# Kernel tuning notes

Measured on AMD Instinct MI355X. Metric: run time of the kernel, lower is better.

## Reference

```python
import jax, jax.numpy as jnp
import numpy as np
import math

L, B, T, D, H, DH, DM, V = 4, 1, 2048, 1024, 16, 64, 4096, 32000
K_TOP = 512
EPS = 1e-6


def setup_inputs() -> dict:
    key = jax.random.key(0)
    ks = jax.random.split(key, 8)
    s = 0.02
    sp = 0.02 / math.sqrt(2 * L)  # c_proj special init
    return {
        "idx": jax.random.randint(ks[0], (B, T), 0, V),
        "wte": jax.random.normal(ks[1], (V, D), jnp.float32) * s,
        "wpe": jax.random.normal(ks[2], (T, D), jnp.float32) * s,
        "ln1_w": jnp.ones((L, D), jnp.float32),
        "ln2_w": jnp.ones((L, D), jnp.float32),
        "W_attn": jax.random.normal(ks[3], (L, D, 3 * H * DH), jnp.float32) * s,
        "W_attn_proj": jax.random.normal(ks[4], (L, H * DH, D), jnp.float32) * sp,
        "W_fc": jax.random.normal(ks[5], (L, D, DM), jnp.float32) * s,
        "W_mlp_proj": jax.random.normal(ks[6], (L, DM, D), jnp.float32) * sp,
        "sink_logit": jnp.zeros((L, H), jnp.float32),
        "lnf_w": jnp.ones((D,), jnp.float32),
        "lm_head_w": jax.random.normal(ks[7], (D, V), jnp.float32) * s,
        "k_topk": K_TOP,
    }


def rmsnorm(x, w):
    return x * jax.lax.rsqrt(jnp.mean(x * x, axis=-1, keepdims=True) + EPS) * w


def abs_topk(x, k):
    # zero all but the k largest-magnitude entries along the last axis
    if k >= x.shape[-1]:
        return x
    vals = jax.lax.top_k(jnp.abs(x), k)[0]
    thresh = vals[..., -1:]
    return jnp.where(jnp.abs(x) >= thresh, x, jnp.zeros((), x.dtype))


def attention_with_sink(xn, Wa, Wap, sink, causal):
    b, t, _ = xn.shape
    qkv = xn @ Wa  # [B,T,3*H*DH]
    q, k, v = jnp.split(qkv, 3, axis=-1)
    q = q.reshape(b, t, H, DH).transpose(0, 2, 1, 3)  # [B,H,T,DH]
    k = k.reshape(b, t, H, DH).transpose(0, 2, 1, 3)
    v = v.reshape(b, t, H, DH).transpose(0, 2, 1, 3)
    scale = 1.0 / math.sqrt(DH)
    scores = jnp.einsum('bhqd,bhkd->bhqk', q, k) * scale
    neg = jnp.finfo(scores.dtype).min
    scores = jnp.where(causal, scores, neg)
    # sink: zero key/value slot at position 0, logit = per-head learnable bias
    sink_col = jnp.broadcast_to(sink[None, :, None, None], (b, H, t, 1)).astype(scores.dtype)
    logits = jnp.concatenate([sink_col, scores], axis=-1)  # [B,H,T,T+1]
    probs = jax.nn.softmax(logits, axis=-1)
    y = jnp.einsum('bhqk,bhkd->bhqd', probs[..., 1:], v)  # sink v is zero
    y = y.transpose(0, 2, 1, 3).reshape(b, t, H * DH)
    return y @ Wap


def reference(idx, wte, wpe, ln1_w, ln2_w, W_attn, W_attn_proj, W_fc, W_mlp_proj,
              sink_logit, lnf_w, lm_head_w, k_topk):
    b, t = idx.shape
    x = wte[idx] + wpe[jnp.arange(t)][None]  # [B,T,D]
    causal = jnp.tril(jnp.ones((t, t), bool))

    def block(x, p):
        l1, l2, Wa, Wap, Wf, Wp, sk = p
        x = x + attention_with_sink(rmsnorm(x, l1), Wa, Wap, sk, causal)
        h = jax.nn.gelu(rmsnorm(x, l2) @ Wf, approximate=False)
        h = abs_topk(h, k_topk)  # AbsTopK at 'mlp_neuron'
        x = x + h @ Wp
        return x, None

    x, _ = jax.lax.scan(block, x, (ln1_w, ln2_w, W_attn, W_attn_proj, W_fc, W_mlp_proj, sink_logit))
    return rmsnorm(x, lnf_w) @ lm_head_w  # [B,T,V]
```

## Files before the change

### kernel.cpp

```cpp
#include <hip/hip_runtime.h>


typedef unsigned int u32;

#define TT 2048
#define DD 1024
#define HH 16
#define DMM 4096
#define VV 32000
#define AQ 4

__global__ __launch_bounds__(256) void embed32_k(const int* __restrict__ idx,
    const float* __restrict__ wte, const float* __restrict__ wpe, float* __restrict__ x){
  int t = blockIdx.x, tid = threadIdx.x;
  int tok = idx[t];
  #pragma unroll
  for (int i=0;i<4;i++){
    int e = tid*4 + i;
    x[(size_t)t*DD + e] = __fadd_rn(wte[(size_t)tok*DD + e], wpe[(size_t)t*DD + e]);
  }
}

__global__ __launch_bounds__(64) void rms_xla_k(const float* __restrict__ x,
    const float* __restrict__ w, float* __restrict__ out){
  __shared__ float sq[1024];
  __shared__ float p5[512];
  __shared__ float fin[64];
  __shared__ float srt;
  int row = blockIdx.x, lane = threadIdx.x;
  const float* xr = x + (size_t)row*DD;
  for (int i=lane; i<1024; i+=64){ float v = xr[i]; sq[i] = __fmul_rn(v,v); }
  __syncthreads();
  for (int t=lane; t<512; t+=64)
    p5[t] = __fadd_rn(sq[2*t], sq[2*t+1]);
  __syncthreads();
  #pragma unroll
  for (int off=32; off; off>>=1){
    for (int t=lane; t<8*off; t+=64){
      int wv = t/off, ii = t - wv*off;
      p5[64*wv+ii] = __fadd_rn(p5[64*wv+ii], p5[64*wv+ii+off]);
    }
    __syncthreads();
  }
  fin[lane] = (lane<8) ? p5[64*lane] : 0.0f;
  __syncthreads();
  #pragma unroll
  for (int off=32; off; off>>=1){
    if (lane<off) fin[lane] = __fadd_rn(fin[lane], fin[lane+off]);
    __syncthreads();
  }
  if (lane==0){
    float mean = __fdiv_rn(fin[0], 1024.0f);
    srt = rsqrtf(__fadd_rn(mean, 1e-6f));
  }
  __syncthreads();
  float r = srt;
  for (int i=lane; i<1024; i+=64)
    out[(size_t)row*DD + i] = __fmul_rn(__fmul_rn(xr[i], r), w[i]);
}

template<int MODE, int NQ>
__global__ __launch_bounds__(256) void gemm_db_k(const float* __restrict__ A,
    const float* __restrict__ B, float* __restrict__ C, int M, int N, int K){
  __shared__ float As[2][16][132];
  __shared__ float Bs[2][16][64*NQ+4];
  const int tid = threadIdx.x;
  const int tr = tid >> 4, tc = tid & 15;
  const int m0 = blockIdx.y*128, n0 = blockIdx.x*(64*NQ);

  const int ar0 = tid >> 2,       af0 = tid & 3;
  const int ar1 = (256+tid) >> 2, af1 = tid & 3;
  float acc[8][4*NQ];
  #pragma unroll
  for (int i=0;i<8;i++)
    #pragma unroll
    for (int j=0;j<4*NQ;j++) acc[i][j] = 0.0f;

  const int niter = K >> 4;
  {
    float4 va0 = *(const float4*)&A[(size_t)(m0+ar0)*K + 4*af0];
    float4 va1 = *(const float4*)&A[(size_t)(m0+ar1)*K + 4*af1];
    As[0][4*af0+0][ar0]=va0.x; As[0][4*af0+1][ar0]=va0.y; As[0][4*af0+2][ar0]=va0.z; As[0][4*af0+3][ar0]=va0.w;
    As[0][4*af1+0][ar1]=va1.x; As[0][4*af1+1][ar1]=va1.y; As[0][4*af1+2][ar1]=va1.z; As[0][4*af1+3][ar1]=va1.w;
    if (NQ==2){
      int r0 = tid>>5, c40 = tid&31;
      int r1 = (256+tid)>>5, c41 = tid&31;
      *(float4*)&Bs[0][r0][4*c40] = *(const float4*)&B[(size_t)r0*N + n0 + 4*c40];
      *(float4*)&Bs[0][r1][4*c41] = *(const float4*)&B[(size_t)r1*N + n0 + 4*c41];
    } else {
      int r0 = tid>>4, c40 = tid&15;
      *(float4*)&Bs[0][r0][4*c40] = *(const float4*)&B[(size_t)r0*N + n0 + 4*c40];
    }
  }
  __syncthreads();

  for (int t=0; t<niter; ++t){
    const int cur = t & 1;
    float4 va0, va1, vb0, vb1;
    if (t+1 < niter){
      int kk = (t+1) << 4;
      va0 = *(const float4*)&A[(size_t)(m0+ar0)*K + kk + 4*af0];
      va1 = *(const float4*)&A[(size_t)(m0+ar1)*K + kk + 4*af1];
      if (NQ==2){
        int r0 = tid>>5, c40 = tid&31;
        int r1 = (256+tid)>>5;
        vb0 = *(const float4*)&B[(size_t)(kk+r0)*N + n0 + 4*c40];
        vb1 = *(const float4*)&B[(size_t)(kk+r1)*N + n0 + 4*c40];
      } else {
        int r0 = tid>>4, c40 = tid&15;
        vb0 = *(const float4*)&B[(size_t)(kk+r0)*N + n0 + 4*c40];
      }
    }
    #pragma unroll 4
    for (int k=0; k<16; ++k){
      float4 a0 = *(const float4*)&As[cur][k][4*tr];
      float4 a1 = *(const float4*)&As[cur][k][64 + 4*tr];
      float4 b0 = *(const float4*)&Bs[cur][k][4*tc];
      float av[8] = {a0.x,a0.y,a0.z,a0.w, a1.x,a1.y,a1.z,a1.w};
      float bv[4*NQ];
      bv[0]=b0.x; bv[1]=b0.y; bv[2]=b0.z; bv[3]=b0.w;
      if (NQ==2){
        float4 b1 = *(const float4*)&Bs[cur][k][64 + 4*tc];
        bv[4]=b1.x; bv[5]=b1.y; bv[6]=b1.z; bv[7]=b1.w;
      }
      #pragma unroll
      for (int i=0;i<8;i++)
        #pragma unroll
        for (int j=0;j<4*NQ;j++)
          acc[i][j] = __builtin_fmaf(av[i], bv[j], acc[i][j]);
    }
    if (t+1 < niter){
      const int nxt = cur ^ 1;
      As[nxt][4*af0+0][ar0]=va0.x; As[nxt][4*af0+1][ar0]=va0.y; As[nxt][4*af0+2][ar0]=va0.z; As[nxt][4*af0+3][ar0]=va0.w;
      As[nxt][4*af1+0][ar1]=va1.x; As[nxt][4*af1+1][ar1]=va1.y; As[nxt][4*af1+2][ar1]=va1.z; As[nxt][4*af1+3][ar1]=va1.w;
      if (NQ==2){
        int r0 = tid>>5, c40 = tid&31;
        int r1 = (256+tid)>>5;
        *(float4*)&Bs[nxt][r0][4*c40] = vb0;
        *(float4*)&Bs[nxt][r1][4*c40] = vb1;
      } else {
        int r0 = tid>>4, c40 = tid&15;
        *(float4*)&Bs[nxt][r0][4*c40] = vb0;
      }
    }
    __syncthreads();
  }

  #pragma unroll
  for (int i=0;i<8;i++){
    int row = m0 + (i>>2)*64 + 4*tr + (i&3);
    #pragma unroll
    for (int jq=0;jq<NQ;jq++){
      size_t off = (size_t)row*N + n0 + jq*64 + 4*tc;
      #pragma unroll
      for (int e=0;e<4;e++){
        float vv = acc[i][jq*4+e];
        if (MODE==0){
          C[off+e] = vv;
        } else if (MODE==1){
          C[off+e] = __fadd_rn(C[off+e], vv);
        } else {
          float t2 = __fdiv_rn(vv, 1.41421356f);
          float g = erff(t2);
          C[off+e] = __fmul_rn(__fmul_rn(0.5f, vv), __fadd_rn(1.0f, g));
        }
      }
    }
  }
}

__global__ __launch_bounds__(256) void attn_v5_k(const float* __restrict__ qkv,
    const float* __restrict__ sink, float* __restrict__ y){
  __shared__ float arr[AQ][2052];
  __shared__ float uks[64*68];
  __shared__ float mq[AQ];
  __shared__ float dq[AQ];
  float (*Ks)[68]   = (float(*)[68])uks;
  float (*p5)[512]  = (float(*)[512])uks;
  float (*fin)[64]  = (float(*)[64])(uks + AQ*512);
  const int tid = threadIdx.x;
  const int lane = tid & 63, wv = tid >> 6;
  const int h = blockIdx.y, q0 = blockIdx.x*AQ;
  const int qa_w = q0 + wv;
  const float snk = sink[h];

  #pragma unroll
  for (int qi=0;qi<AQ;qi++)
    for (int s=tid; s<2052; s+=256) arr[qi][s] = 0.0f;

  float qv[64];
  {
    const float* qr = qkv + (size_t)qa_w*3072 + h*64;
    #pragma unroll
    for (int c4=0;c4<16;c4++){
      float4 v = *(const float4*)&qr[4*c4];
      qv[4*c4]=v.x; qv[4*c4+1]=v.y; qv[4*c4+2]=v.z; qv[4*c4+3]=v.w;
    }
  }

  float ml = -3.402823466e38f;
  const int qmax = q0 + AQ - 1;
  for (int base=0; base<=qmax; base+=64){
    __syncthreads();
    #pragma unroll
    for (int it=0; it<4; ++it){
      int id = it*256 + tid;
      int r = id >> 4, c4 = id & 15;
      int kr = base + r;
      if (kr < TT)
        *(float4*)&Ks[r][4*c4] = *(const float4*)&qkv[(size_t)kr*3072 + 1024 + h*64 + 4*c4];
    }
    __syncthreads();
    int kv = base + lane;
    if (kv <= qa_w){
      float s = 0.0f;
      #pragma unroll
      for (int c4=0;c4<16;c4++){
        float4 kf = *(const float4*)&Ks[lane][4*c4];
        s = __builtin_fmaf(qv[4*c4  ], kf.x, s);
        s = __builtin_fmaf(qv[4*c4+1], kf.y, s);
        s = __builtin_fmaf(qv[4*c4+2], kf.z, s);
        s = __builtin_fmaf(qv[4*c4+3], kf.w, s);
      }
      s = __fmul_rn(s, 0.125f);
      arr[wv][1+kv] = s;
      ml = fmaxf(ml, s);
    }
  }
  #pragma unroll
  for (int off=1; off<64; off<<=1) ml = fmaxf(ml, __shfl_xor(ml, off, 64));
  if (lane==0) mq[wv] = fmaxf(ml, snk);
  __syncthreads();

  #pragma unroll
  for (int qi=0;qi<AQ;qi++){
    float m = mq[qi]; int qa = q0+qi;
    for (int s=tid; s<2049; s+=256){
      if (s >= 1 && s-1 <= qa)
        arr[qi][s] = expf(__fsub_rn(arr[qi][s], m));
    }
  }
  if (tid < AQ) arr[tid][0] = expf(__fsub_rn(snk, mq[tid]));
  __syncthreads();

  #pragma unroll
  for (int m2=0; m2<8; ++m2){
    int flat = m2*256 + tid;
    int qi = flat >> 9, t = flat & 511;
    float a = 0.0f;
    for (int s=t; s<2049; s+=512) a = __fadd_rn(a, arr[qi][s]);
    p5[qi][t] = a;
  }
  __syncthreads();
  #pragma unroll
  for (int off=32; off; off>>=1){
    for (int t=tid; t<AQ*8*off; t+=256){
      int qi = t/(8*off); int rem = t - qi*8*off;
      int g = rem/off, ii = rem - g*off;
      p5[qi][64*g+ii] = __fadd_rn(p5[qi][64*g+ii], p5[qi][64*g+ii+off]);
    }
    __syncthreads();
  }
  { int qi = tid>>6, i = tid&63; fin[qi][i] = (i<8) ? p5[qi][64*i] : 0.0f; }
  __syncthreads();
  #pragma unroll
  for (int off=32; off; off>>=1){
    for (int t=tid; t<AQ*off; t+=256){
      int qi = t/off, ii = t - qi*off;
      fin[qi][ii] = __fadd_rn(fin[qi][ii], fin[qi][ii+off]);
    }
    __syncthreads();
  }
  if (tid < AQ) dq[tid] = fin[tid][0];
  __syncthreads();

  #pragma unroll
  for (int qi=0;qi<AQ;qi++){
    float den = dq[qi]; int qa = q0+qi;
    for (int s=tid; s<2049; s+=256)
      if (s >= 1 && s-1 <= qa)
        arr[qi][s] = __fdiv_rn(arr[qi][s], den);
  }
  __syncthreads();

  const int d = lane;
  float acc = 0.0f;
  const float* vb = qkv + 2048 + h*64 + d;
  int kv = 0;
  for (; kv + 8 <= qa_w + 1; kv += 8){
    #pragma unroll
    for (int e=0;e<8;e++)
      acc = __builtin_fmaf(arr[wv][1+kv+e], vb[(size_t)(kv+e)*3072], acc);
  }
  for (; kv <= qa_w; ++kv)
    acc = __builtin_fmaf(arr[wv][1+kv], vb[(size_t)kv*3072], acc);
  y[(size_t)qa_w*DD + h*64 + d] = acc;
}

__global__ __launch_bounds__(256) void topk32_k(float* __restrict__ h,
    const int* __restrict__ kptr){
  const int row = blockIdx.x, tid = threadIdx.x;
  __shared__ int suf[256];
  __shared__ int s_sel, s_k;
  float* hr = h + (size_t)row*DMM;
  int kk = kptr[0];
  u32 prefix = 0u;
  for (int pass=0; pass<4; pass++){
    int shift = 24 - 8*pass;
    u32 hi_mask = pass ? (0xFFFFFFFFu << (shift+8)) : 0u;
    suf[tid] = 0;
    __syncthreads();
    for (int i=0;i<16;i++){
      u32 b = __float_as_uint(hr[tid + 256*i]) & 0x7fffffffu;
      if ((b & hi_mask) == prefix) atomicAdd(&suf[(b>>shift)&255], 1);
    }
    __syncthreads();
    for (int s=1;s<256;s<<=1){
      int v2 = (tid+s<256) ? suf[tid+s] : 0;
      __syncthreads();
      suf[tid] += v2;
      __syncthreads();
    }
    int nxt = (tid<255) ? suf[tid+1] : 0;
    if (suf[tid] >= kk && nxt < kk){ s_sel = tid; s_k = kk - nxt; }
    __syncthreads();
    prefix |= ((u32)s_sel) << shift;
    kk = s_k;
    __syncthreads();
  }
  for (int i=0;i<16;i++){
    int e = tid + 256*i;
    u32 b = __float_as_uint(hr[e]) & 0x7fffffffu;
    if (b < prefix) hr[e] = 0.0f;
  }
}

extern "C" void kernel_launch(void* const* d_in, const int* in_sizes, int n_in,
                              void* d_out, int out_size, void* d_ws, size_t ws_size,
                              hipStream_t stream){
  const int*   idx  = (const int*)  d_in[0];
  const float* wte  = (const float*)d_in[1];
  const float* wpe  = (const float*)d_in[2];
  const float* ln1  = (const float*)d_in[3];
  const float* ln2  = (const float*)d_in[4];
  const float* Wa   = (const float*)d_in[5];
  const float* Wap  = (const float*)d_in[6];
  const float* Wf   = (const float*)d_in[7];
  const float* Wp   = (const float*)d_in[8];
  const float* sink = (const float*)d_in[9];
  const float* lnf  = (const float*)d_in[10];
  const float* lmw  = (const float*)d_in[11];
  const int*   kptr = (const int*)  d_in[12];
  (void)in_sizes; (void)n_in; (void)out_size; (void)ws_size;

  char* w = (char*)d_ws;
  float* x   = (float*)(w);
  float* xn  = (float*)(w + 8388608);
  float* qkv = (float*)(w + 16777216);
  float* y   = (float*)(w + 41943040);
  float* h   = (float*)(w + 50331648);

  embed32_k<<<TT, 256, 0, stream>>>(idx, wte, wpe, x);

  for (int l=0; l<4; l++){
    rms_xla_k<<<TT, 64, 0, stream>>>(x, ln1 + l*DD, xn);
    gemm_db_k<0,2><<<dim3(3072/128, TT/128), 256, 0, stream>>>(xn, Wa + (size_t)l*1024*3072, qkv, TT, 3072, 1024);
    attn_v5_k<<<dim3(TT/AQ, HH), 256, 0, stream>>>(qkv, sink + l*HH, y);
    gemm_db_k<1,1><<<dim3(1024/64, TT/128), 256, 0, stream>>>(y, Wap + (size_t)l*1024*1024, x, TT, 1024, 1024);
    rms_xla_k<<<TT, 64, 0, stream>>>(x, ln2 + l*DD, xn);
    gemm_db_k<2,2><<<dim3(4096/128, TT/128), 256, 0, stream>>>(xn, Wf + (size_t)l*1024*4096, h, TT, 4096, 1024);
    topk32_k<<<TT, 256, 0, stream>>>(h, kptr);
    gemm_db_k<1,1><<<dim3(1024/64, TT/128), 256, 0, stream>>>(h, Wp + (size_t)l*4096*1024, x, TT, 1024, 4096);
  }

  rms_xla_k<<<TT, 64, 0, stream>>>(x, lnf, xn);
  gemm_db_k<0,2><<<dim3(VV/128, TT/128), 256, 0, stream>>>(xn, lmw, (float*)d_out, TT, VV, 1024);
}
```

Before: 8.001 ms.

## Stage V tiles in shared memory and use per-wave softmax reductions

The attention kernel now loads V in 64-row tiles into shared memory, shared by the block's four query waves. Before, each wave read V straight from global memory with strided loads. The softmax normalisation is also rewritten so each wave handles its own query row. It uses wave shuffles for the max and sum instead of block-wide shared-memory tree reductions with many __syncthreads. The summation order is kept close to the original, at the cost of extra block barriers in the new V-tile loop.

Result: no change. 7.866 ms (-1.7%).

```diff
diff --git a/kernel.cpp b/kernel.cpp
--- a/kernel.cpp
+++ b/kernel.cpp
@@ -169,24 +169,20 @@
   }
 }
 
-__global__ __launch_bounds__(256) void attn_v5_k(const float* __restrict__ qkv,
+__global__ __launch_bounds__(256) void attn_v6_k(const float* __restrict__ qkv,
     const float* __restrict__ sink, float* __restrict__ y){
-  __shared__ float arr[AQ][2052];
-  __shared__ float uks[64*68];
-  __shared__ float mq[AQ];
-  __shared__ float dq[AQ];
-  float (*Ks)[68]   = (float(*)[68])uks;
-  float (*p5)[512]  = (float(*)[512])uks;
-  float (*fin)[64]  = (float(*)[64])(uks + AQ*512);
+  __shared__ float arr[AQ][2049];
+  __shared__ float Ks[64][68];
   const int tid = threadIdx.x;
   const int lane = tid & 63, wv = tid >> 6;
   const int h = blockIdx.y, q0 = blockIdx.x*AQ;
   const int qa_w = q0 + wv;
+  const int qmax = q0 + AQ - 1;
   const float snk = sink[h];
 
   #pragma unroll
   for (int qi=0;qi<AQ;qi++)
-    for (int s=tid; s<2052; s+=256) arr[qi][s] = 0.0f;
+    for (int s=tid; s<2049; s+=256) arr[qi][s] = 0.0f;
 
   float qv[64];
   {
@@ -199,7 +195,6 @@
   }
 
   float ml = -3.402823466e38f;
-  const int qmax = q0 + AQ - 1;
   for (int base=0; base<=qmax; base+=64){
     __syncthreads();
     #pragma unroll
@@ -227,74 +222,66 @@
       ml = fmaxf(ml, s);
     }
   }
+  __syncthreads();
+
   #pragma unroll
   for (int off=1; off<64; off<<=1) ml = fmaxf(ml, __shfl_xor(ml, off, 64));
-  if (lane==0) mq[wv] = fmaxf(ml, snk);
-  __syncthreads();
-
-  #pragma unroll
-  for (int qi=0;qi<AQ;qi++){
-    float m = mq[qi]; int qa = q0+qi;
-    for (int s=tid; s<2049; s+=256){
-      if (s >= 1 && s-1 <= qa)
-        arr[qi][s] = expf(__fsub_rn(arr[qi][s], m));
-    }
-  }
-  if (tid < AQ) arr[tid][0] = expf(__fsub_rn(snk, mq[tid]));
-  __syncthreads();
-
-  #pragma unroll
-  for (int m2=0; m2<8; ++m2){
-    int flat = m2*256 + tid;
-    int qi = flat >> 9, t = flat & 511;
+  float m = fmaxf(ml, snk);
+
+  for (int s=1+lane; s<=1+qa_w; s+=64)
+    arr[wv][s] = expf(__fsub_rn(arr[wv][s], m));
+  if (lane==0) arr[wv][0] = expf(__fsub_rn(snk, m));
+
+  float pg[8];
+  #pragma unroll
+  for (int g=0; g<8; ++g){
+    int t = lane + 64*g;
     float a = 0.0f;
-    for (int s=t; s<2049; s+=512) a = __fadd_rn(a, arr[qi][s]);
-    p5[qi][t] = a;
-  }
-  __syncthreads();
-  #pragma unroll
-  for (int off=32; off; off>>=1){
-    for (int t=tid; t<AQ*8*off; t+=256){
-      int qi = t/(8*off); int rem = t - qi*8*off;
-      int g = rem/off, ii = rem - g*off;
-      p5[qi][64*g+ii] = __fadd_rn(p5[qi][64*g+ii], p5[qi][64*g+ii+off]);
-    }
-    __syncthreads();
-  }
-  { int qi = tid>>6, i = tid&63; fin[qi][i] = (i<8) ? p5[qi][64*i] : 0.0f; }
-  __syncthreads();
-  #pragma unroll
-  for (int off=32; off; off>>=1){
-    for (int t=tid; t<AQ*off; t+=256){
-      int qi = t/off, ii = t - qi*off;
-      fin[qi][ii] = __fadd_rn(fin[qi][ii], fin[qi][ii+off]);
-    }
-    __syncthreads();
-  }
-  if (tid < AQ) dq[tid] = fin[tid][0];
-  __syncthreads();
-
-  #pragma unroll
-  for (int qi=0;qi<AQ;qi++){
-    float den = dq[qi]; int qa = q0+qi;
-    for (int s=tid; s<2049; s+=256)
-      if (s >= 1 && s-1 <= qa)
-        arr[qi][s] = __fdiv_rn(arr[qi][s], den);
-  }
-  __syncthreads();
-
-  const int d = lane;
+    for (int s=t; s<2049; s+=512) a = __fadd_rn(a, arr[wv][s]);
+    pg[g] = a;
+  }
+  #pragma unroll
+  for (int g=0; g<8; ++g){
+    #pragma unroll
+    for (int off=32; off; off>>=1)
+      pg[g] = __fadd_rn(pg[g], __shfl_down(pg[g], off, 64));
+  }
+  float den;
+  {
+    float t04 = __fadd_rn(pg[0], pg[4]);
+    float t26 = __fadd_rn(pg[2], pg[6]);
+    float t15 = __fadd_rn(pg[1], pg[5]);
+    float t37 = __fadd_rn(pg[3], pg[7]);
+    float d0 = __fadd_rn(__fadd_rn(t04, t26), __fadd_rn(t15, t37));
+    den = __shfl(d0, 0, 64);
+  }
+
+  for (int s=1+lane; s<=1+qa_w; s+=64)
+    arr[wv][s] = __fdiv_rn(arr[wv][s], den);
+
   float acc = 0.0f;
-  const float* vb = qkv + 2048 + h*64 + d;
-  int kv = 0;
-  for (; kv + 8 <= qa_w + 1; kv += 8){
-    #pragma unroll
-    for (int e=0;e<8;e++)
-      acc = __builtin_fmaf(arr[wv][1+kv+e], vb[(size_t)(kv+e)*3072], acc);
-  }
-  for (; kv <= qa_w; ++kv)
-    acc = __builtin_fmaf(arr[wv][1+kv], vb[(size_t)kv*3072], acc);
-  y[(size_t)qa_w*DD + h*64 + d] = acc;
+  for (int base=0; base<=qmax; base+=64){
+    __syncthreads();
+    #pragma unroll
+    for (int it=0; it<4; ++it){
+      int id = it*256 + tid;
+      int r = id >> 4, c4 = id & 15;
+      int kr = base + r;
+      if (kr < TT)
+        *(float4*)&Ks[r][4*c4] = *(const float4*)&qkv[(size_t)kr*3072 + 2048 + h*64 + 4*c4];
+    }
+    __syncthreads();
+    int lim = qa_w - base; if (lim > 63) lim = 63;
+    int j = 0;
+    for (; j + 8 <= lim + 1; j += 8){
+      #pragma unroll
+      for (int e=0;e<8;e++)
+        acc = __builtin_fmaf(arr[wv][1+base+j+e], Ks[j+e][lane], acc);
+    }
+    for (; j <= lim; ++j)
+      acc = __builtin_fmaf(arr[wv][1+base+j], Ks[j][lane], acc);
+  }
+  y[(size_t)qa_w*DD + h*64 + lane] = acc;
 }
 
 __global__ __launch_bounds__(256) void topk32_k(float* __restrict__ h,
@@ -365,7 +352,7 @@
   for (int l=0; l<4; l++){
     rms_xla_k<<<TT, 64, 0, stream>>>(x, ln1 + l*DD, xn);
     gemm_db_k<0,2><<<dim3(3072/128, TT/128), 256, 0, stream>>>(xn, Wa + (size_t)l*1024*3072, qkv, TT, 3072, 1024);
-    attn_v5_k<<<dim3(TT/AQ, HH), 256, 0, stream>>>(qkv, sink + l*HH, y);
+    attn_v6_k<<<dim3(TT/AQ, HH), 256, 0, stream>>>(qkv, sink + l*HH, y);
     gemm_db_k<1,1><<<dim3(1024/64, TT/128), 256, 0, stream>>>(y, Wap + (size_t)l*1024*1024, x, TT, 1024, 1024);
     rms_xla_k<<<TT, 64, 0, stream>>>(x, ln2 + l*DD, xn);
     gemm_db_k<2,2><<<dim3(4096/128, TT/128), 256, 0, stream>>>(xn, Wf + (size_t)l*1024*4096, h, TT, 4096, 1024);
```
